# Kernel optimization log

Hardware: AMD Instinct MI355X
Metric: run time of the kernel (lower is better)

The kernel has to match this reference:

```python
import jax, jax.numpy as jnp
import numpy as np

BS, C, H, W = 8, 64, 256, 256
N_MODE_1, N_MODE_2 = 32, 32  # retained modes along H-rfft and W-rfft


def setup_inputs() -> dict:
    key = jax.random.key(0)
    ks = jax.random.split(key, 5)
    ci = co = C // 2
    scale = 1.0 / (C * C)  # module's self.scale flavor; kaiming init approximated by scaled normal
    return {
        "x": jax.random.normal(ks[0], (BS, C, H, W), jnp.float32),
        "w1_re": jax.random.normal(ks[1], (2, ci, co, N_MODE_1), jnp.float32) * 0.05,
        "w1_im": jax.random.normal(ks[2], (2, ci, co, N_MODE_1), jnp.float32) * 0.05,
        "w2_re": jax.random.normal(ks[3], (2, ci, co, N_MODE_2), jnp.float32) * 0.05,
        "w2_im": jax.random.normal(ks[4], (2, ci, co, N_MODE_2), jnp.float32) * 0.05,
    }


def reference(x, w1_re, w1_im, w2_re, w2_im):
    bs, c, h, w = x.shape
    x5 = x.reshape(bs, 2, c // 2, h, w)  # split channels into 2 groups

    # ---- spectral conv along W (dim=-1), weight_2 ----
    w2c = w2_re + 1j * w2_im  # [2, ci, co, n_mode_2]
    x_ft = jnp.fft.rfft(x5, axis=-1, norm="ortho")  # [bs,2,ci,h,w//2+1]
    out_ft = jnp.einsum("bgixy,gioy->bgoxy", x_ft[..., :N_MODE_2], w2c)
    out_ft = jnp.pad(out_ft, ((0, 0), (0, 0), (0, 0), (0, 0), (0, x_ft.shape[-1] - N_MODE_2)))
    x5 = jnp.fft.irfft(out_ft, n=w, axis=-1, norm="ortho")

    # ---- spectral conv along H (dim=-2), weight_1 ----
    w1c = w1_re + 1j * w1_im  # [2, ci, co, n_mode_1]
    x_ft = jnp.fft.rfft(x5, axis=-2, norm="ortho")  # [bs,2,ci,h//2+1,w]
    out_ft = jnp.einsum("bgixy,giox->bgoxy", x_ft[..., :N_MODE_1, :], w1c)
    out_ft = jnp.pad(out_ft, ((0, 0), (0, 0), (0, 0), (0, x_ft.shape[-2] - N_MODE_1), (0, 0)))
    x5 = jnp.fft.irfft(out_ft, n=h, axis=-2, norm="ortho")

    return x5.reshape(bs, c, h, w)
```

## Files before the change

kernel.cpp:

```cpp
#include <hip/hip_runtime.h>
#include <math.h>

#define PI2_256 0.0245436926061702596754894014318f
#define TS 260

__global__ __launch_bounds__(256) void init_tab(float* __restrict__ tc, float* __restrict__ ts) {
    int idx = blockIdx.x * 256 + threadIdx.x;
    int k = idx >> 8, n = idx & 255;
    int m = (k * n) & 255;
    float s, c;
    sincosf(PI2_256 * (float)m, &s, &c);
    tc[idx] = c;
    ts[idx] = s;
}

__global__ __launch_bounds__(256) void w_fwd(const float* __restrict__ x,
                                             const float* __restrict__ w2r,
                                             const float* __restrict__ w2i,
                                             float* __restrict__ Yw) {
    __shared__ float tile[32 * TS];
    __shared__ float XrL[32 * 36], XiL[32 * 36];

    const int bid  = blockIdx.x;
    const int xrow = bid & 255;
    const int g    = (bid >> 8) & 1;
    const int b    = bid >> 9;
    const int t    = threadIdx.x;

    const size_t chan0 = (size_t)(b * 64 + g * 32);
    const size_t base  = (chan0 * 256 + xrow) * 256;

    {
        const int wq = t & 63, i0 = t >> 6;
        #pragma unroll
        for (int r = 0; r < 8; ++r) {
            const int i = i0 + r * 4;
            *(float4*)(tile + i * TS + wq * 4) =
                *(const float4*)(x + base + (size_t)i * 65536 + wq * 4);
        }
    }
    __syncthreads();

    {
        const int hq = t & 31, i0 = t >> 5;
        const int h0 = hq * 4;
        float4 A[4], B[4]; float c0[4], x128v[4];
        #pragma unroll
        for (int r = 0; r < 4; ++r) {
            const float* row = tile + (i0 + r * 8) * TS;
            A[r] = *(const float4*)(row + h0);
            B[r] = *(const float4*)(row + 4 * (63 - hq));
            x128v[r] = row[128];
        }
        #pragma unroll
        for (int r = 0; r < 4; ++r) {
            const float up = __shfl_up(B[r].x, 1);
            c0[r] = (hq == 0) ? A[r].x : up;
        }
        __syncthreads();
        #pragma unroll
        for (int r = 0; r < 4; ++r) {
            float* row = tile + (i0 + r * 8) * TS;
            float4 ye = make_float4(A[r].x + c0[r], A[r].y + B[r].w,
                                    A[r].z + B[r].z, A[r].w + B[r].y);
            float4 yo = make_float4(A[r].x - c0[r], A[r].y - B[r].w,
                                    A[r].z - B[r].z, A[r].w - B[r].y);
            if (hq == 0) yo.x = x128v[r];
            *(float4*)(row + h0)       = ye;
            *(float4*)(row + 128 + h0) = yo;
        }
    }
    __syncthreads();

    {
        const int hs = t & 1;
        const int kg = (t >> 1) & 7;
        const int rg = t >> 4;
        const float* rp0 = tile + (2 * rg) * TS;
        const float* rp1 = rp0 + TS;
        const float sgn = (kg & 1) ? -1.f : 1.f;
        const int hb = hs * 64;

        float cA[4], sA[4], cB[4], sB[4], t2[4];
        float xr[4][2], xi[4][2];
        #pragma unroll
        for (int kk = 0; kk < 4; ++kk) {
            const int k = kg + 8 * kk;
            float sd, cd; sincosf(PI2_256 * (float)k, &sd, &cd);
            t2[kk] = 2.f * cd;
            float ss, cc;
            sincosf(PI2_256 * (float)((k * hb) & 255), &ss, &cc);
            cA[kk] = cc; sA[kk] = ss;
            sincosf(PI2_256 * (float)((k * (hb - 1)) & 255), &ss, &cc);
            cB[kk] = cc; sB[kk] = ss;
        }
        const float x0_0 = rp0[0] * 0.5f, x128_0 = rp0[128];
        const float x0_1 = rp1[0] * 0.5f, x128_1 = rp1[128];
        #pragma unroll
        for (int kk = 0; kk < 4; ++kk) {
            xr[kk][0] = (hs == 0) ? (sgn * x128_0 - x0_0) : 0.f;
            xr[kk][1] = (hs == 0) ? (sgn * x128_1 - x0_1) : 0.f;
            xi[kk][0] = 0.f; xi[kk][1] = 0.f;
        }
        for (int hq = 0; hq < 16; ++hq) {
            const float4 ye0 = *(const float4*)(rp0 + hb + hq * 4);
            const float4 yo0 = *(const float4*)(rp0 + 128 + hb + hq * 4);
            const float4 ye1 = *(const float4*)(rp1 + hb + hq * 4);
            const float4 yo1 = *(const float4*)(rp1 + 128 + hb + hq * 4);
            #pragma unroll
            for (int j = 0; j < 4; ++j) {
                const float e0 = (&ye0.x)[j], o0 = (&yo0.x)[j];
                const float e1 = (&ye1.x)[j], o1 = (&yo1.x)[j];
                #pragma unroll
                for (int kk = 0; kk < 4; ++kk) {
                    xr[kk][0] += e0 * cA[kk];  xi[kk][0] -= o0 * sA[kk];
                    xr[kk][1] += e1 * cA[kk];  xi[kk][1] -= o1 * sA[kk];
                    const float cn = t2[kk] * cA[kk] - cB[kk]; cB[kk] = cA[kk]; cA[kk] = cn;
                    const float sn = t2[kk] * sA[kk] - sB[kk]; sB[kk] = sA[kk]; sA[kk] = sn;
                }
            }
        }
        #pragma unroll
        for (int kk = 0; kk < 4; ++kk)
            #pragma unroll
            for (int r = 0; r < 2; ++r) {
                xr[kk][r] += __shfl_xor(xr[kk][r], 1);
                xi[kk][r] += __shfl_xor(xi[kk][r], 1);
            }
        if (hs == 0) {
            #pragma unroll
            for (int kk = 0; kk < 4; ++kk) {
                const int k = kg + 8 * kk;
                XrL[(2 * rg    ) * 36 + k] = xr[kk][0];
                XiL[(2 * rg    ) * 36 + k] = xi[kk][0];
                XrL[(2 * rg + 1) * 36 + k] = xr[kk][1];
                XiL[(2 * rg + 1) * 36 + k] = xi[kk][1];
            }
        }
    }
    __syncthreads();

    {
        const int kq = t & 7, o = t >> 3;
        const int k4 = kq * 4;
        float4 ar = {0,0,0,0}, ai = {0,0,0,0};
        const float* wrb = w2r + (size_t)g * 32768 + o * 32 + k4;
        const float* wib = w2i + (size_t)g * 32768 + o * 32 + k4;
        for (int i = 0; i < 32; ++i) {
            const float4 xr = *(const float4*)(XrL + i * 36 + k4);
            const float4 xi = *(const float4*)(XiL + i * 36 + k4);
            const float4 wr = *(const float4*)(wrb + i * 1024);
            const float4 wi = *(const float4*)(wib + i * 1024);
            ar.x += xr.x * wr.x - xi.x * wi.x;  ai.x += xr.x * wi.x + xi.x * wr.x;
            ar.y += xr.y * wr.y - xi.y * wi.y;  ai.y += xr.y * wi.y + xi.y * wr.y;
            ar.z += xr.z * wr.z - xi.z * wi.z;  ai.z += xr.z * wi.z + xi.z * wr.z;
            ar.w += xr.w * wr.w - xi.w * wi.w;  ai.w += xr.w * wi.w + xi.w * wr.w;
        }
        const float s2 = 2.f / 256.f, s1 = 1.f / 256.f;
        const float s0 = (k4 == 0) ? s1 : s2;
        float* dst = Yw + (size_t)((b * 2 + g) * 32 + o) * 16384 + (size_t)xrow * 64 + k4;
        *(float4*)(dst)      = make_float4(ar.x * s0, ar.y * s2, ar.z * s2, ar.w * s2);
        *(float4*)(dst + 32) = make_float4(ai.x * s0, ai.y * s2, ai.z * s2, ai.w * s2);
    }
}

__global__ __launch_bounds__(256) void h_fwd(const float* __restrict__ Yw,
                                             float* __restrict__ Z) {
    __shared__ float YL[256 * 64];
    const int bid = blockIdx.x;
    const int t = threadIdx.x;
    {
        const float* src = Yw + (size_t)bid * 16384;
        #pragma unroll
        for (int r = 0; r < 16; ++r) {
            const int f = t + r * 256;
            *(float4*)(YL + f * 4) = *(const float4*)(src + f * 4);
        }
    }
    __syncthreads();

    const int hs = t & 1, kg = (t >> 1) & 7, sp = t >> 4;
    const int hb = hs * 64;
    const float sgn = (kg & 1) ? -1.f : 1.f;
    const float4 y0q   = *(const float4*)(YL + sp * 4);
    const float4 y128q = *(const float4*)(YL + 128 * 64 + sp * 4);

    float cA[4], sA[4], cB[4], sB[4], t2[4];
    float xr[4][4], xi[4][4];
    #pragma unroll
    for (int kk = 0; kk < 4; ++kk) {
        const int k = kg + 8 * kk;
        float sd, cd; sincosf(PI2_256 * (float)k, &sd, &cd);
        t2[kk] = 2.f * cd;
        float ss, cc;
        sincosf(PI2_256 * (float)((k * hb) & 255), &ss, &cc);
        cA[kk] = cc; sA[kk] = ss;
        sincosf(PI2_256 * (float)((k * (hb - 1)) & 255), &ss, &cc);
        cB[kk] = cc; sB[kk] = ss;
        #pragma unroll
        for (int j = 0; j < 4; ++j) {
            xr[kk][j] = (hs == 0) ? (sgn * (&y128q.x)[j] - (&y0q.x)[j]) : 0.f;
            xi[kk][j] = 0.f;
        }
    }
    for (int h = hb; h < hb + 64; ++h) {
        const float4 aq = *(const float4*)(YL + h * 64 + sp * 4);
        const float4 mq = *(const float4*)(YL + ((256 - h) & 255) * 64 + sp * 4);
        float ye[4], yo[4];
        #pragma unroll
        for (int j = 0; j < 4; ++j) {
            ye[j] = (&aq.x)[j] + (&mq.x)[j];
            yo[j] = (&aq.x)[j] - (&mq.x)[j];
        }
        #pragma unroll
        for (int kk = 0; kk < 4; ++kk) {
            #pragma unroll
            for (int j = 0; j < 4; ++j) {
                xr[kk][j] += ye[j] * cA[kk];
                xi[kk][j] -= yo[j] * sA[kk];
            }
            const float cn = t2[kk] * cA[kk] - cB[kk]; cB[kk] = cA[kk]; cA[kk] = cn;
            const float sn = t2[kk] * sA[kk] - sB[kk]; sB[kk] = sA[kk]; sA[kk] = sn;
        }
    }
    #pragma unroll
    for (int kk = 0; kk < 4; ++kk)
        #pragma unroll
        for (int j = 0; j < 4; ++j) {
            xr[kk][j] += __shfl_xor(xr[kk][j], 1);
            xi[kk][j] += __shfl_xor(xi[kk][j], 1);
        }
    if (hs == 0) {
        const int o = bid & 31, bg = bid >> 5;
        #pragma unroll
        for (int kk = 0; kk < 4; ++kk) {
            const int k = kg + 8 * kk;
            const size_t zi_ = (((size_t)bg * 32 + k) * 32 + o) * 128 + sp * 4;
            *(float4*)(Z + zi_)      = make_float4(xr[kk][0], xr[kk][1], xr[kk][2], xr[kk][3]);
            *(float4*)(Z + zi_ + 64) = make_float4(xi[kk][0], xi[kk][1], xi[kk][2], xi[kk][3]);
        }
    }
}

__global__ __launch_bounds__(256) void h_mix2(const float* __restrict__ Z,
                                              const float* __restrict__ w1r,
                                              const float* __restrict__ w1i,
                                              float* __restrict__ Z2) {
    __shared__ float ZL[32 * 128];
    __shared__ float WrL[1024], WiL[1024];
    const int bid = blockIdx.x;
    const int kh = bid & 31, bg = bid >> 5;
    const int g = bg & 1;
    const int t = threadIdx.x;
    {
        const float* src = Z + (size_t)bid * 4096;
        #pragma unroll
        for (int r = 0; r < 4; ++r) {
            const int f = t + r * 256;
            *(float4*)(ZL + f * 4) = *(const float4*)(src + f * 4);
        }
        #pragma unroll
        for (int r = 0; r < 4; ++r) {
            const int idx = t + r * 256;
            const int gidx = g * 32768 + (idx >> 5) * 1024 + (idx & 31) * 32 + kh;
            WrL[idx] = w1r[gidx];
            WiL[idx] = w1i[gidx];
        }
    }
    __syncthreads();

    const int s = t & 63, og = t >> 6;
    float accr[8], acci[8];
    #pragma unroll
    for (int m = 0; m < 8; ++m) { accr[m] = 0.f; acci[m] = 0.f; }
    for (int i = 0; i < 32; ++i) {
        const float zr = ZL[i * 128 + s];
        const float zi = ZL[i * 128 + 64 + s];
        #pragma unroll
        for (int m = 0; m < 8; ++m) {
            const int o = og * 8 + m;
            const float wr = WrL[i * 32 + o];
            const float wi = WiL[i * 32 + o];
            accr[m] += zr * wr - zi * wi;
            acci[m] += zr * wi + zi * wr;
        }
    }
    const float sck = (kh == 0) ? (1.f / 256.f) : (2.f / 256.f);
    #pragma unroll
    for (int m = 0; m < 8; ++m) {
        const int o = og * 8 + m;
        const size_t zo = ((size_t)(bg * 32 + o) * 32 + kh) * 128 + s;
        Z2[zo]      = accr[m] * sck;
        Z2[zo + 64] = acci[m] * sck;
    }
}

__global__ __launch_bounds__(256) void h_inv2(const float* __restrict__ Z2,
                                              const float* __restrict__ tc,
                                              const float* __restrict__ ts,
                                              float* __restrict__ YHg) {
    __shared__ float ZL[32 * 128];
    __shared__ float TcL[32 * 128], TsL[32 * 128];
    const int bid = blockIdx.x;
    const int t = threadIdx.x;
    {
        const float* src = Z2 + (size_t)bid * 4096;
        #pragma unroll
        for (int r = 0; r < 4; ++r) {
            const int f = t + r * 256;
            *(float4*)(ZL + f * 4) = *(const float4*)(src + f * 4);
        }
        #pragma unroll
        for (int r = 0; r < 4; ++r) {
            const int q = t + r * 256;
            const int k = q >> 5, hq = q & 31;
            *(float4*)(TcL + k * 128 + hq * 4) = *(const float4*)(tc + (size_t)k * 256 + hq * 4);
            *(float4*)(TsL + k * 128 + hq * 4) = *(const float4*)(ts + (size_t)k * 256 + hq * 4);
        }
    }
    __syncthreads();

    const int s = t & 63, hg = t >> 6;
    float zr[32], zi[32];
    #pragma unroll
    for (int k = 0; k < 32; ++k) {
        zr[k] = ZL[k * 128 + s];
        zi[k] = ZL[k * 128 + 64 + s];
    }
    float* dst = YHg + (size_t)bid * 16384;
    #pragma unroll
    for (int jq = 0; jq < 8; ++jq) {
        const int h0 = hg * 32 + jq * 4;
        float sC[4] = {0, 0, 0, 0}, sS[4] = {0, 0, 0, 0};
        #pragma unroll
        for (int k = 0; k < 32; ++k) {
            const float4 c4 = *(const float4*)(TcL + k * 128 + h0);
            const float4 s4 = *(const float4*)(TsL + k * 128 + h0);
            sC[0] += zr[k] * c4.x;  sS[0] += zi[k] * s4.x;
            sC[1] += zr[k] * c4.y;  sS[1] += zi[k] * s4.y;
            sC[2] += zr[k] * c4.z;  sS[2] += zi[k] * s4.z;
            sC[3] += zr[k] * c4.w;  sS[3] += zi[k] * s4.w;
        }
        #pragma unroll
        for (int jj = 0; jj < 4; ++jj) {
            const int h = h0 + jj;
            dst[h * 64 + s] = sC[jj] - sS[jj];
            if (h > 0) dst[(256 - h) * 64 + s] = sC[jj] + sS[jj];
        }
    }
    if (hg == 0) {
        float ny = 0.f;
        #pragma unroll
        for (int k = 0; k < 32; ++k) ny += (k & 1) ? -zr[k] : zr[k];
        dst[128 * 64 + s] = ny;
    }
}

__global__ __launch_bounds__(256) void w_inv2(const float* __restrict__ YHg,
                                              const float* __restrict__ tc,
                                              const float* __restrict__ ts,
                                              float* __restrict__ out) {
    __shared__ float YL[32 * 64];
    __shared__ float TcL[32 * 128], TsL[32 * 128];
    const int bid = blockIdx.x;
    const int hb = bid & 7, c = bid >> 3;
    const int t = threadIdx.x;
    {
        const float* src = YHg + (size_t)c * 16384 + hb * 2048;
        #pragma unroll
        for (int r = 0; r < 2; ++r) {
            const int f = t + r * 256;
            *(float4*)(YL + f * 4) = *(const float4*)(src + f * 4);
        }
        #pragma unroll
        for (int r = 0; r < 4; ++r) {
            const int q = t + r * 256;
            const int k = q >> 5, wq_ = q & 31;
            *(float4*)(TcL + k * 128 + wq_ * 4) = *(const float4*)(tc + (size_t)k * 256 + wq_ * 4);
            *(float4*)(TsL + k * 128 + wq_ * 4) = *(const float4*)(ts + (size_t)k * 256 + wq_ * 4);
        }
    }
    __syncthreads();

    const int wq = t & 31, hh = t >> 5;
    const int w0 = wq * 4;
    float* outp = out + (size_t)c * 65536;

    float sC[4][4], sS[4][4];
    float nyA[4];
    #pragma unroll
    for (int j = 0; j < 4; ++j) {
        nyA[j] = 0.f;
        #pragma unroll
        for (int jj = 0; jj < 4; ++jj) { sC[j][jj] = 0.f; sS[j][jj] = 0.f; }
    }

    for (int k = 0; k < 32; ++k) {
        const float4 c4 = *(const float4*)(TcL + k * 128 + w0);
        const float4 s4 = *(const float4*)(TsL + k * 128 + w0);
        const float sk = (k & 1) ? -1.f : 1.f;
        #pragma unroll
        for (int j = 0; j < 4; ++j) {
            const int hl = hh * 4 + j;
            const float R = YL[hl * 64 + k];
            const float I = YL[hl * 64 + 32 + k];
            nyA[j] += sk * R;
            sC[j][0] += R * c4.x;  sS[j][0] += I * s4.x;
            sC[j][1] += R * c4.y;  sS[j][1] += I * s4.y;
            sC[j][2] += R * c4.z;  sS[j][2] += I * s4.z;
            sC[j][3] += R * c4.w;  sS[j][3] += I * s4.w;
        }
    }
    #pragma unroll
    for (int j = 0; j < 4; ++j) {
        const int h = hb * 32 + hh * 4 + j;
        *(float4*)(outp + (size_t)h * 256 + w0) =
            make_float4(sC[j][0] - sS[j][0], sC[j][1] - sS[j][1],
                        sC[j][2] - sS[j][2], sC[j][3] - sS[j][3]);
        const float p0 = sC[j][0] + sS[j][0];
        const float p1 = sC[j][1] + sS[j][1];
        const float p2 = sC[j][2] + sS[j][2];
        const float p3 = sC[j][3] + sS[j][3];
        const float m0s = __shfl(p0, 32 - wq, 32);
        const float m0  = (wq == 0) ? nyA[j] : m0s;
        const float m1  = __shfl(p3, 31 - wq, 32);
        const float m2  = __shfl(p2, 31 - wq, 32);
        const float m3  = __shfl(p1, 31 - wq, 32);
        *(float4*)(outp + (size_t)h * 256 + 128 + w0) = make_float4(m0, m1, m2, m3);
    }
}

extern "C" void kernel_launch(void* const* d_in, const int* in_sizes, int n_in,
                              void* d_out, int out_size, void* d_ws, size_t ws_size,
                              hipStream_t stream) {
    const float* x   = (const float*)d_in[0];
    const float* w1r = (const float*)d_in[1];
    const float* w1i = (const float*)d_in[2];
    const float* w2r = (const float*)d_in[3];
    const float* w2i = (const float*)d_in[4];
    float* out = (float*)d_out;
    float* ws  = (float*)d_ws;

    float* tc = ws;
    float* ts = ws + 8192;
    float* Yw = ws + 16384;
    float* Z  = Yw + 8388608;
    float* Z2 = Z + 2097152;

    init_tab<<<32, 256, 0, stream>>>(tc, ts);
    w_fwd<<<4096, 256, 0, stream>>>(x, w2r, w2i, Yw);
    h_fwd<<<512, 256, 0, stream>>>(Yw, Z);
    h_mix2<<<512, 256, 0, stream>>>(Z, w1r, w1i, Z2);
    h_inv2<<<512, 256, 0, stream>>>(Z2, tc, ts, Yw);
    w_inv2<<<4096, 256, 0, stream>>>(Yw, tc, ts, out);
}
```

Measured before the change: 192.9 us.

## Compute W-direction forward DFT with split-bf16 MFMA against precomputed twiddle table

The scalar Chebyshev-recurrence DFT along W in w_fwd is replaced by a matrix multiply on MFMA bf16 instructions. The input rows and a precomputed 64x256 cos/-sin table are each split into high and low bf16 parts, and three MFMA products recover near-fp32 accuracy. A new init kernel builds the table. Separately, h_fwd now reads per-block sincos values from a small shared table and uses exact quarter-turn start values, removing most of its transcendental calls. The risks are accuracy loss from the three-term bf16 split and extra LDS traffic for the split operands.

```diff
diff --git a/kernel.cpp b/kernel.cpp
--- a/kernel.cpp
+++ b/kernel.cpp
@@ -2,7 +2,18 @@
 #include <math.h>
 
 #define PI2_256 0.0245436926061702596754894014318f
-#define TS 260
+
+typedef __attribute__((ext_vector_type(8))) short short8;
+typedef __attribute__((ext_vector_type(4))) float f32x4;
+
+static __device__ __forceinline__ unsigned short f2bf(float f) {
+    unsigned int u = __float_as_uint(f);
+    u = (u + 0x7FFFu + ((u >> 16) & 1u)) >> 16;
+    return (unsigned short)u;
+}
+static __device__ __forceinline__ float bf2f(unsigned short h) {
+    return __uint_as_float(((unsigned int)h) << 16);
+}
 
 __global__ __launch_bounds__(256) void init_tab(float* __restrict__ tc, float* __restrict__ ts) {
     int idx = blockIdx.x * 256 + threadIdx.x;
@@ -14,11 +25,28 @@
     ts[idx] = s;
 }
 
+__global__ __launch_bounds__(256) void init_et(unsigned short* __restrict__ Eth,
+                                               unsigned short* __restrict__ Etl) {
+    int idx = blockIdx.x * 256 + threadIdx.x;
+    int n = idx >> 8, w = idx & 255;
+    int k = n & 31;
+    int m = (k * w) & 255;
+    float s, c;
+    sincosf(PI2_256 * (float)m, &s, &c);
+    float v = (n < 32) ? c : -s;
+    unsigned short h = f2bf(v);
+    Eth[idx] = h;
+    Etl[idx] = f2bf(v - bf2f(h));
+}
+
 __global__ __launch_bounds__(256) void w_fwd(const float* __restrict__ x,
                                              const float* __restrict__ w2r,
                                              const float* __restrict__ w2i,
+                                             const unsigned short* __restrict__ Eth,
+                                             const unsigned short* __restrict__ Etl,
                                              float* __restrict__ Yw) {
-    __shared__ float tile[32 * TS];
+    __shared__ __attribute__((aligned(16))) unsigned short Ah[32 * 256];
+    __shared__ __attribute__((aligned(16))) unsigned short Al[32 * 256];
     __shared__ float XrL[32 * 36], XiL[32 * 36];
 
     const int bid  = blockIdx.x;
@@ -35,106 +63,61 @@
         #pragma unroll
         for (int r = 0; r < 8; ++r) {
             const int i = i0 + r * 4;
-            *(float4*)(tile + i * TS + wq * 4) =
-                *(const float4*)(x + base + (size_t)i * 65536 + wq * 4);
-        }
-    }
-    __syncthreads();
-
-    {
-        const int hq = t & 31, i0 = t >> 5;
-        const int h0 = hq * 4;
-        float4 A[4], B[4]; float c0[4], x128v[4];
-        #pragma unroll
-        for (int r = 0; r < 4; ++r) {
-            const float* row = tile + (i0 + r * 8) * TS;
-            A[r] = *(const float4*)(row + h0);
-            B[r] = *(const float4*)(row + 4 * (63 - hq));
-            x128v[r] = row[128];
-        }
-        #pragma unroll
-        for (int r = 0; r < 4; ++r) {
-            const float up = __shfl_up(B[r].x, 1);
-            c0[r] = (hq == 0) ? A[r].x : up;
-        }
-        __syncthreads();
-        #pragma unroll
-        for (int r = 0; r < 4; ++r) {
-            float* row = tile + (i0 + r * 8) * TS;
-            float4 ye = make_float4(A[r].x + c0[r], A[r].y + B[r].w,
-                                    A[r].z + B[r].z, A[r].w + B[r].y);
-            float4 yo = make_float4(A[r].x - c0[r], A[r].y - B[r].w,
-                                    A[r].z - B[r].z, A[r].w - B[r].y);
-            if (hq == 0) yo.x = x128v[r];
-            *(float4*)(row + h0)       = ye;
-            *(float4*)(row + 128 + h0) = yo;
-        }
-    }
-    __syncthreads();
-
-    {
-        const int hs = t & 1;
-        const int kg = (t >> 1) & 7;
-        const int rg = t >> 4;
-        const float* rp0 = tile + (2 * rg) * TS;
-        const float* rp1 = rp0 + TS;
-        const float sgn = (kg & 1) ? -1.f : 1.f;
-        const int hb = hs * 64;
-
-        float cA[4], sA[4], cB[4], sB[4], t2[4];
-        float xr[4][2], xi[4][2];
-        #pragma unroll
-        for (int kk = 0; kk < 4; ++kk) {
-            const int k = kg + 8 * kk;
-            float sd, cd; sincosf(PI2_256 * (float)k, &sd, &cd);
-            t2[kk] = 2.f * cd;
-            float ss, cc;
-            sincosf(PI2_256 * (float)((k * hb) & 255), &ss, &cc);
-            cA[kk] = cc; sA[kk] = ss;
-            sincosf(PI2_256 * (float)((k * (hb - 1)) & 255), &ss, &cc);
-            cB[kk] = cc; sB[kk] = ss;
-        }
-        const float x0_0 = rp0[0] * 0.5f, x128_0 = rp0[128];
-        const float x0_1 = rp1[0] * 0.5f, x128_1 = rp1[128];
-        #pragma unroll
-        for (int kk = 0; kk < 4; ++kk) {
-            xr[kk][0] = (hs == 0) ? (sgn * x128_0 - x0_0) : 0.f;
-            xr[kk][1] = (hs == 0) ? (sgn * x128_1 - x0_1) : 0.f;
-            xi[kk][0] = 0.f; xi[kk][1] = 0.f;
-        }
-        for (int hq = 0; hq < 16; ++hq) {
-            const float4 ye0 = *(const float4*)(rp0 + hb + hq * 4);
-            const float4 yo0 = *(const float4*)(rp0 + 128 + hb + hq * 4);
-            const float4 ye1 = *(const float4*)(rp1 + hb + hq * 4);
-            const float4 yo1 = *(const float4*)(rp1 + 128 + hb + hq * 4);
-            #pragma unroll
-            for (int j = 0; j < 4; ++j) {
-                const float e0 = (&ye0.x)[j], o0 = (&yo0.x)[j];
-                const float e1 = (&ye1.x)[j], o1 = (&yo1.x)[j];
-                #pragma unroll
-                for (int kk = 0; kk < 4; ++kk) {
-                    xr[kk][0] += e0 * cA[kk];  xi[kk][0] -= o0 * sA[kk];
-                    xr[kk][1] += e1 * cA[kk];  xi[kk][1] -= o1 * sA[kk];
-                    const float cn = t2[kk] * cA[kk] - cB[kk]; cB[kk] = cA[kk]; cA[kk] = cn;
-                    const float sn = t2[kk] * sA[kk] - sB[kk]; sB[kk] = sA[kk]; sA[kk] = sn;
-                }
+            const float4 v = *(const float4*)(x + base + (size_t)i * 65536 + wq * 4);
+            ushort4 hq, lq;
+            {
+                const float f0 = v.x, f1 = v.y, f2 = v.z, f3 = v.w;
+                hq.x = f2bf(f0); lq.x = f2bf(f0 - bf2f(hq.x));
+                hq.y = f2bf(f1); lq.y = f2bf(f1 - bf2f(hq.y));
+                hq.z = f2bf(f2); lq.z = f2bf(f2 - bf2f(hq.z));
+                hq.w = f2bf(f3); lq.w = f2bf(f3 - bf2f(hq.w));
             }
-        }
-        #pragma unroll
-        for (int kk = 0; kk < 4; ++kk)
-            #pragma unroll
-            for (int r = 0; r < 2; ++r) {
-                xr[kk][r] += __shfl_xor(xr[kk][r], 1);
-                xi[kk][r] += __shfl_xor(xi[kk][r], 1);
-            }
-        if (hs == 0) {
-            #pragma unroll
-            for (int kk = 0; kk < 4; ++kk) {
-                const int k = kg + 8 * kk;
-                XrL[(2 * rg    ) * 36 + k] = xr[kk][0];
-                XiL[(2 * rg    ) * 36 + k] = xi[kk][0];
-                XrL[(2 * rg + 1) * 36 + k] = xr[kk][1];
-                XiL[(2 * rg + 1) * 36 + k] = xi[kk][1];
+            *(ushort4*)(Ah + i * 256 + wq * 4) = hq;
+            *(ushort4*)(Al + i * 256 + wq * 4) = lq;
+        }
+    }
+    __syncthreads();
+
+    {
+        const int l  = t & 63, wv = t >> 6;
+        const int lr = l & 15, lk = (l >> 4) * 8;
+        f32x4 acc0 = {0.f, 0.f, 0.f, 0.f};
+        f32x4 acc1 = {0.f, 0.f, 0.f, 0.f};
+        const unsigned short* bhp = Eth + (size_t)(wv * 16 + lr) * 256 + lk;
+        const unsigned short* blp = Etl + (size_t)(wv * 16 + lr) * 256 + lk;
+        const unsigned short* a0p = Ah + lr * 256 + lk;
+        const unsigned short* a1p = Ah + (16 + lr) * 256 + lk;
+        const unsigned short* c0p = Al + lr * 256 + lk;
+        const unsigned short* c1p = Al + (16 + lr) * 256 + lk;
+        #pragma unroll
+        for (int ks = 0; ks < 8; ++ks) {
+            const int off = ks * 32;
+            const short8 bh = *(const short8*)(bhp + off);
+            const short8 bl = *(const short8*)(blp + off);
+            const short8 a0 = *(const short8*)(a0p + off);
+            const short8 a1 = *(const short8*)(a1p + off);
+            const short8 c0 = *(const short8*)(c0p + off);
+            const short8 c1 = *(const short8*)(c1p + off);
+            acc0 = __builtin_amdgcn_mfma_f32_16x16x32_bf16(a0, bh, acc0, 0, 0, 0);
+            acc1 = __builtin_amdgcn_mfma_f32_16x16x32_bf16(a1, bh, acc1, 0, 0, 0);
+            acc0 = __builtin_amdgcn_mfma_f32_16x16x32_bf16(a0, bl, acc0, 0, 0, 0);
+            acc1 = __builtin_amdgcn_mfma_f32_16x16x32_bf16(a1, bl, acc1, 0, 0, 0);
+            acc0 = __builtin_amdgcn_mfma_f32_16x16x32_bf16(c0, bh, acc0, 0, 0, 0);
+            acc1 = __builtin_amdgcn_mfma_f32_16x16x32_bf16(c1, bh, acc1, 0, 0, 0);
+        }
+        const int col   = wv * 16 + lr;
+        const int rbase = (l >> 4) * 4;
+        #pragma unroll
+        for (int r = 0; r < 4; ++r) {
+            const int row0 = rbase + r;
+            const int row1 = 16 + rbase + r;
+            const float v0 = acc0[r], v1 = acc1[r];
+            if (col < 32) {
+                XrL[row0 * 36 + col] = v0;
+                XrL[row1 * 36 + col] = v1;
+            } else {
+                XiL[row0 * 36 + col - 32] = v0;
+                XiL[row1 * 36 + col - 32] = v1;
             }
         }
     }
@@ -167,8 +150,13 @@
 __global__ __launch_bounds__(256) void h_fwd(const float* __restrict__ Yw,
                                              float* __restrict__ Z) {
     __shared__ float YL[256 * 64];
+    __shared__ float kC[32], kS[32];
     const int bid = blockIdx.x;
     const int t = threadIdx.x;
+    if (t < 32) {
+        float s, c; sincosf(PI2_256 * (float)t, &s, &c);
+        kC[t] = c; kS[t] = s;
+    }
     {
         const float* src = Yw + (size_t)bid * 16384;
         #pragma unroll
@@ -190,13 +178,18 @@
     #pragma unroll
     for (int kk = 0; kk < 4; ++kk) {
         const int k = kg + 8 * kk;
-        float sd, cd; sincosf(PI2_256 * (float)k, &sd, &cd);
+        const float cd = kC[k], sd = kS[k];
         t2[kk] = 2.f * cd;
-        float ss, cc;
-        sincosf(PI2_256 * (float)((k * hb) & 255), &ss, &cc);
-        cA[kk] = cc; sA[kk] = ss;
-        sincosf(PI2_256 * (float)((k * (hb - 1)) & 255), &ss, &cc);
-        cB[kk] = cc; sB[kk] = ss;
+        float cA0, sA0;
+        if (hs == 0) { cA0 = 1.f; sA0 = 0.f; }
+        else {
+            const int km = k & 3;
+            cA0 = (km == 0) ? 1.f : (km == 2) ? -1.f : 0.f;
+            sA0 = (km == 1) ? 1.f : (km == 3) ? -1.f : 0.f;
+        }
+        cA[kk] = cA0; sA[kk] = sA0;
+        cB[kk] = cA0 * cd + sA0 * sd;
+        sB[kk] = sA0 * cd - cA0 * sd;
         #pragma unroll
         for (int j = 0; j < 4; ++j) {
             xr[kk][j] = (hs == 0) ? (sgn * (&y128q.x)[j] - (&y0q.x)[j]) : 0.f;
@@ -446,9 +439,12 @@
     float* Yw = ws + 16384;
     float* Z  = Yw + 8388608;
     float* Z2 = Z + 2097152;
+    unsigned short* Eth = (unsigned short*)(Z2 + 2097152);
+    unsigned short* Etl = Eth + 16384;
 
     init_tab<<<32, 256, 0, stream>>>(tc, ts);
-    w_fwd<<<4096, 256, 0, stream>>>(x, w2r, w2i, Yw);
+    init_et<<<64, 256, 0, stream>>>(Eth, Etl);
+    w_fwd<<<4096, 256, 0, stream>>>(x, w2r, w2i, Eth, Etl, Yw);
     h_fwd<<<512, 256, 0, stream>>>(Yw, Z);
     h_mix2<<<512, 256, 0, stream>>>(Z, w1r, w1i, Z2);
     h_inv2<<<512, 256, 0, stream>>>(Z2, tc, ts, Yw);
```

Measured after the change: 203.5 us. 5.5% more time.
